# Kernel optimization log

Hardware: AMD Instinct MI355X
Metric: run time of the kernel (lower is better)

The kernel has to match this reference:

```python
import jax, jax.numpy as jnp
import numpy as np

HEADS = 16
EMBED = 1024
D_K = EMBED // HEADS


def setup_inputs() -> dict:
    key = jax.random.key(0)
    ks = jax.random.split(key, 11)
    B, S, E = 4, 2048, EMBED
    sc = 0.02
    return {
        "query": jax.random.normal(ks[0], (B, S, E), jnp.float32),
        "key_": jax.random.normal(ks[1], (B, S, E), jnp.float32),
        "value": jax.random.normal(ks[2], (B, S, E), jnp.float32),
        "Wq": jax.random.normal(ks[3], (E, E), jnp.float32) * sc,
        "bq": jnp.zeros((E,), jnp.float32),
        "Wk": jax.random.normal(ks[4], (E, E), jnp.float32) * sc,
        "bk": jnp.zeros((E,), jnp.float32),
        "Wv": jax.random.normal(ks[5], (E, E), jnp.float32) * sc,
        "bv": jnp.zeros((E,), jnp.float32),
        "Wo": jax.random.normal(ks[6], (E, D_K), jnp.float32) * sc,  # out: Linear(heads*d_k -> d_k)
        "bo": jnp.zeros((D_K,), jnp.float32),
    }


def reference(query, key_, value, Wq, bq, Wk, bk, Wv, bv, Wo, bo):
    B, S, E = query.shape
    H, Dk = HEADS, D_K
    # QKV projections
    q = query @ Wq + bq          # (B,S,E)
    k = key_ @ Wk + bk
    v = value @ Wv + bv
    # split heads -> (B,H,S,Dk)
    q = q.reshape(B, S, H, Dk).transpose(0, 2, 1, 3)
    k = k.reshape(B, S, H, Dk).transpose(0, 2, 1, 3)
    v = v.reshape(B, S, H, Dk).transpose(0, 2, 1, 3)
    # attention: softmax(QK^T / sqrt(d_k)) V
    scores = jnp.einsum("bhqd,bhkd->bhqk", q, k) / jnp.sqrt(jnp.asarray(Dk, q.dtype))
    attn = jax.nn.softmax(scores, axis=-1)
    ctx = jnp.einsum("bhqk,bhkd->bhqd", attn, v)
    ctx = ctx.transpose(0, 2, 1, 3).reshape(B, S, E)
    # output projection (E -> d_k, as in source)
    return ctx @ Wo + bo
```

## Files before the change

### kernel.cpp

```cpp
#include <hip/hip_runtime.h>
#include <hip/hip_bf16.h>
#include <cstdint>
#include <cstddef>

#define DEVI static __device__ __forceinline__

typedef unsigned short u16;
typedef unsigned int u32;
typedef __bf16 bf16_t;
typedef __bf16 bf16x8 __attribute__((ext_vector_type(8)));
typedef float f32x4 __attribute__((ext_vector_type(4)));
typedef float f32x16 __attribute__((ext_vector_type(16)));

union U16x8 { uint4 u; bf16x8 v; };
union PU { u32 w[4]; bf16x8 v; };

#define QSCALE 0.1803368801111204f

DEVI void gload_lds16(const void* g, void* l) {
  __builtin_amdgcn_global_load_lds((const __attribute__((address_space(1))) void*)g,
                                   (__attribute__((address_space(3))) void*)l, 16, 0, 0);
}
DEVI void wait_vmcnt0() { asm volatile("s_waitcnt vmcnt(0)" ::: "memory"); }

DEVI u32 cvt_pk_bf16(float lo, float hi) {
  u32 r;
  asm("v_cvt_pk_bf16_f32 %0, %1, %2" : "=v"(r) : "v"(lo), "v"(hi));
  return r;
}

DEVI void permswap(u32& a, u32& b) {
  asm("v_permlane32_swap_b32 %0, %1" : "+v"(a), "+v"(b));
}

DEVI f32x16 mfma32(bf16x8 a, bf16x8 b, f32x16 c) {
  return __builtin_amdgcn_mfma_f32_32x32x16_bf16(a, b, c, 0, 0, 0);
}

DEVI bf16x8 lds_frag(const char* base, int row, int koff, int swz) {
  U16x8 u;
  u.u = *(const uint4*)(base + row * 128 + (koff ^ swz));
  return u.v;
}

DEVI void transpose_body(const float* __restrict__ src, bf16_t* __restrict__ dst,
                         int R, int C, float scale, int tile, int t,
                         u16 (*tileb)[65]) {
  int tiles_c = C >> 6;
  int tc = tile % tiles_c;
  int tr = tile / tiles_c;
  int r0 = tr << 6, c0 = tc << 6;
  #pragma unroll
  for (int p = 0; p < 4; ++p) {
    int idx = t + p * 256;
    int i = idx >> 4, j4 = (idx & 15) * 4;
    float4 f = *(const float4*)(src + (size_t)(r0 + i) * C + c0 + j4);
    tileb[i][j4 + 0] = __builtin_bit_cast(u16, (bf16_t)(f.x * scale));
    tileb[i][j4 + 1] = __builtin_bit_cast(u16, (bf16_t)(f.y * scale));
    tileb[i][j4 + 2] = __builtin_bit_cast(u16, (bf16_t)(f.z * scale));
    tileb[i][j4 + 3] = __builtin_bit_cast(u16, (bf16_t)(f.w * scale));
  }
  __syncthreads();
  #pragma unroll
  for (int p = 0; p < 2; ++p) {
    int idx = t + p * 256;
    int j = idx >> 3, i0 = (idx & 7) * 8;
    u16 us[8];
    #pragma unroll
    for (int e = 0; e < 8; ++e) us[e] = tileb[i0 + e][j];
    uint4 o;
    o.x = (u32)us[0] | ((u32)us[1] << 16);
    o.y = (u32)us[2] | ((u32)us[3] << 16);
    o.z = (u32)us[4] | ((u32)us[5] << 16);
    o.w = (u32)us[6] | ((u32)us[7] << 16);
    *(uint4*)((u16*)dst + (size_t)(c0 + j) * R + r0 + i0) = o;
  }
}

__global__ __launch_bounds__(256) void k_prep(
    const float* __restrict__ qa, const float* __restrict__ ka, const float* __restrict__ va,
    const float* __restrict__ Wq, const float* __restrict__ Wk,
    const float* __restrict__ Wv, const float* __restrict__ Wo,
    bf16_t* __restrict__ Abf,
    bf16_t* __restrict__ WqT, bf16_t* __restrict__ WkT,
    bf16_t* __restrict__ WvT, bf16_t* __restrict__ WoT) {
  __shared__ u16 tileb[64][65];
  const int bid = blockIdx.x;
  const int t = threadIdx.x;
  if (bid < 3072) {
    int which = bid >> 10;
    int bb = bid & 1023;
    const float* s = which == 0 ? qa : which == 1 ? ka : va;
    u16* d = (u16*)Abf + (size_t)which * 8192 * 1024;
    size_t base = ((size_t)bb * 256 + t) * 8;
    #pragma unroll
    for (int p = 0; p < 4; ++p) {
      size_t i = base + (size_t)p * 2097152;
      float4 f0 = *(const float4*)(s + i);
      float4 f1 = *(const float4*)(s + i + 4);
      uint4 o;
      o.x = cvt_pk_bf16(f0.x, f0.y); o.y = cvt_pk_bf16(f0.z, f0.w);
      o.z = cvt_pk_bf16(f1.x, f1.y); o.w = cvt_pk_bf16(f1.z, f1.w);
      *(uint4*)(d + i) = o;
    }
  } else {
    int r = bid - 3072;
    if (r < 256)      transpose_body(Wq, WqT, 1024, 1024, QSCALE, r,       t, tileb);
    else if (r < 512) transpose_body(Wk, WkT, 1024, 1024, 1.0f,   r - 256, t, tileb);
    else if (r < 768) transpose_body(Wv, WvT, 1024, 1024, 1.0f,   r - 512, t, tileb);
    else              transpose_body(Wo, WoT, 1024, 64,   1.0f,   r - 768, t, tileb);
  }
}

template<bool PRE>
__global__ __launch_bounds__(256) void k_proj_gemm(
    const float* __restrict__ Aq, const float* __restrict__ Ak, const float* __restrict__ Av,
    const bf16_t* __restrict__ Abf,
    const bf16_t* __restrict__ WqT, const bf16_t* __restrict__ WkT, const bf16_t* __restrict__ WvT,
    const float* __restrict__ bq, const float* __restrict__ bk, const float* __restrict__ bv,
    bf16_t* __restrict__ qh, bf16_t* __restrict__ kh, bf16_t* __restrict__ vT) {
  int bx = blockIdx.x;
  int which = bx >> 9;
  int tt = bx & 511;
  int tile_m = tt & 63;
  int tile_n = tt >> 6;
  const float* A    = which == 0 ? Aq : which == 1 ? Ak : Av;
  const bf16_t* Ab  = Abf + (size_t)which * 8192 * 1024;
  const bf16_t* WT  = which == 0 ? WqT : which == 1 ? WkT : WvT;
  const float* bias = which == 0 ? bq : which == 1 ? bk : bv;
  const float bscale = which == 0 ? QSCALE : 1.0f;

  const int t = threadIdx.x;
  const int l = t & 63;
  const int w = t >> 6;
  const int wm = w >> 1, wn = w & 1;
  const int c = l & 15, g = l >> 4;
  const int row0 = tile_m << 7;
  const int n0 = tile_n << 7;

  __shared__ __align__(16) char As[128 * 64 * 2];
  __shared__ __align__(16) char Bs[128 * 64 * 2];

  f32x4 acc[4][4];
  #pragma unroll
  for (int i = 0; i < 4; ++i)
    #pragma unroll
    for (int j = 0; j < 4; ++j) acc[i][j] = (f32x4){0.f, 0.f, 0.f, 0.f};

  const int arow_b = t >> 4, ac4 = t & 15;
  const float* agbase = A + (size_t)(row0 + arow_b) * 1024 + ac4 * 4;
  char* aldst = As + arow_b * 128 + (((ac4 >> 1) ^ (arow_b & 7)) << 4) + (ac4 & 1) * 8;

  for (int kt = 0; kt < 16; ++kt) {
    __syncthreads();
    if constexpr (PRE) {
      #pragma unroll
      for (int cc = 0; cc < 4; ++cc) {
        int slot = w * 256 + cc * 64 + l;
        int row = slot >> 3, chs = slot & 7;
        const bf16_t* src = Ab + (size_t)(row0 + row) * 1024 + kt * 64 + ((chs ^ (row & 7)) << 3);
        gload_lds16(src, As + (w * 256 + cc * 64) * 16);
      }
    } else {
      const float* ap = agbase + kt * 64;
      #pragma unroll
      for (int p = 0; p < 8; ++p) {
        float4 f = *(const float4*)(ap + (size_t)p * 16384);
        uint2 o;
        o.x = cvt_pk_bf16(f.x, f.y);
        o.y = cvt_pk_bf16(f.z, f.w);
        *(uint2*)(aldst + p * 2048) = o;
      }
    }
    #pragma unroll
    for (int cc = 0; cc < 4; ++cc) {
      int slot = w * 256 + cc * 64 + l;
      int row = slot >> 3, chs = slot & 7;
      const bf16_t* src = WT + (size_t)(n0 + row) * 1024 + kt * 64 + ((chs ^ (row & 7)) << 3);
      gload_lds16(src, Bs + (w * 256 + cc * 64) * 16);
    }
    wait_vmcnt0();
    __syncthreads();
    #pragma unroll
    for (int kk = 0; kk < 2; ++kk) {
      bf16x8 af[4], bfr[4];
      #pragma unroll
      for (int mi = 0; mi < 4; ++mi) {
        int row = wm * 64 + mi * 16 + c;
        U16x8 u; u.u = *(const uint4*)(As + row * 128 + ((kk * 64 + g * 16) ^ ((c & 7) << 4)));
        af[mi] = u.v;
      }
      #pragma unroll
      for (int ni = 0; ni < 4; ++ni) {
        int row = wn * 64 + ni * 16 + c;
        U16x8 u; u.u = *(const uint4*)(Bs + row * 128 + ((kk * 64 + g * 16) ^ ((c & 7) << 4)));
        bfr[ni] = u.v;
      }
      #pragma unroll
      for (int mi = 0; mi < 4; ++mi)
        #pragma unroll
        for (int ni = 0; ni < 4; ++ni)
          acc[mi][ni] = __builtin_amdgcn_mfma_f32_16x16x32_bf16(af[mi], bfr[ni], acc[mi][ni], 0, 0, 0);
    }
  }

  const int b = row0 >> 11;
  const int sl0 = row0 & 2047;
  if (which == 2) {
    u16* vbase = (u16*)vT;
    #pragma unroll
    for (int ni = 0; ni < 4; ++ni) {
      int col = n0 + wn * 64 + ni * 16 + c;
      float bb = bias[col];
      int h = col >> 6, d = col & 63;
      u16* rowp = vbase + (((size_t)(b * 16 + h) * 64 + d) * 2048);
      #pragma unroll
      for (int mi = 0; mi < 4; ++mi) {
        int s = sl0 + wm * 64 + mi * 16 + g * 4;
        uint2 pv;
        pv.x = cvt_pk_bf16(acc[mi][ni][0] + bb, acc[mi][ni][1] + bb);
        pv.y = cvt_pk_bf16(acc[mi][ni][2] + bb, acc[mi][ni][3] + bb);
        *(uint2*)(rowp + s) = pv;
      }
    }
  } else {
    bf16_t* dst = which == 0 ? qh : kh;
    u16* dd = (u16*)dst;
    #pragma unroll
    for (int ni = 0; ni < 4; ++ni) {
      int col = n0 + wn * 64 + ni * 16 + c;
      float bb = bias[col] * bscale;
      int h = col >> 6, d = col & 63;
      #pragma unroll
      for (int mi = 0; mi < 4; ++mi) {
        #pragma unroll
        for (int r = 0; r < 4; ++r) {
          int s = sl0 + wm * 64 + mi * 16 + g * 4 + r;
          float vv = acc[mi][ni][r] + bb;
          size_t idx = (((size_t)b * 16 + h) * 2048 + s) * 64 + d;
          dd[idx] = __builtin_bit_cast(u16, (bf16_t)vv);
        }
      }
    }
  }
}

__global__ __launch_bounds__(256, 4) void k_attn(
    const bf16_t* __restrict__ qh, const bf16_t* __restrict__ kh,
    const bf16_t* __restrict__ vT, bf16_t* __restrict__ ctx) {
  const int bid = blockIdx.x;
  const int bx = ((bid & 7) << 7) | (bid >> 3);
  const int bh = bx >> 4;
  const int qt = bx & 15;
  const int q0 = qt << 7;
  const int t = threadIdx.x, l = t & 63, w = t >> 6;
  const int q = l & 31;
  const int hi = l >> 5;
  const int swz = (q & 7) << 4;

  __shared__ __align__(16) char Ks[2][64 * 128];
  __shared__ __align__(16) char Vs[2][64 * 128];

  const u16* qrow = (const u16*)qh + ((size_t)bh * 2048 + q0 + w * 32 + q) * 64;
  bf16x8 qf0, qf1, qf2, qf3;
  {
    U16x8 u;
    u.u = *(const uint4*)(qrow + 0 * 16 + hi * 8); qf0 = u.v;
    u.u = *(const uint4*)(qrow + 1 * 16 + hi * 8); qf1 = u.v;
    u.u = *(const uint4*)(qrow + 2 * 16 + hi * 8); qf2 = u.v;
    u.u = *(const uint4*)(qrow + 3 * 16 + hi * 8); qf3 = u.v;
  }

  bf16x8 ones;
  {
    U16x8 u;
    u.u = (uint4){0x3F803F80u, 0x3F803F80u, 0x3F803F80u, 0x3F803F80u};
    ones = u.v;
  }

  const f32x16 z16 = {0.f,0.f,0.f,0.f, 0.f,0.f,0.f,0.f, 0.f,0.f,0.f,0.f, 0.f,0.f,0.f,0.f};
  f32x16 oc0 = z16, oc1 = z16, psum = z16;

  const u16* kbh = (const u16*)kh + (size_t)bh * 2048 * 64;
  const u16* vbh = (const u16*)vT + (size_t)bh * 64 * 2048;

  auto stage = [&](int kvi, int buf) {
    int kbase = kvi << 6;
    #pragma unroll
    for (int cc = 0; cc < 2; ++cc) {
      int slot = w * 128 + cc * 64 + l;
      int row = slot >> 3, chs = slot & 7;
      gload_lds16(kbh + (size_t)(kbase + row) * 64 + ((chs ^ (row & 7)) << 3),
                  Ks[buf] + (w * 128 + cc * 64) * 16);
      gload_lds16(vbh + (size_t)row * 2048 + kbase + ((chs ^ (row & 7)) << 3),
                  Vs[buf] + (w * 128 + cc * 64) * 16);
    }
  };

  stage(0, 0);
  wait_vmcnt0();
  __syncthreads();

  for (int kv = 0; kv < 32; ++kv) {
    const int cur = kv & 1;
    if (kv < 31) stage(kv + 1, cur ^ 1);
    const char* Kc = Ks[cur];
    const char* Vc = Vs[cur];

    #pragma unroll
    for (int tt = 0; tt < 2; ++tt) {
      const int arow = tt * 32 + q;
      f32x16 st = z16;
      __builtin_amdgcn_s_setprio(1);
      st = mfma32(lds_frag(Kc, arow, 0 * 32 + hi * 16, swz), qf0, st);
      st = mfma32(lds_frag(Kc, arow, 1 * 32 + hi * 16, swz), qf1, st);
      st = mfma32(lds_frag(Kc, arow, 2 * 32 + hi * 16, swz), qf2, st);
      st = mfma32(lds_frag(Kc, arow, 3 * 32 + hi * 16, swz), qf3, st);
      __builtin_amdgcn_s_setprio(0);

      float e[16];
      #pragma unroll
      for (int i = 0; i < 16; ++i) e[i] = __builtin_amdgcn_exp2f(st[i]);

      #pragma unroll
      for (int cc = 0; cc < 2; ++cc) {
        u32 a  = cvt_pk_bf16(e[8 * cc + 0], e[8 * cc + 1]);
        u32 b  = cvt_pk_bf16(e[8 * cc + 4], e[8 * cc + 5]);
        u32 c2 = cvt_pk_bf16(e[8 * cc + 2], e[8 * cc + 3]);
        u32 d  = cvt_pk_bf16(e[8 * cc + 6], e[8 * cc + 7]);
        permswap(a, b);
        permswap(c2, d);
        PU pu;
        pu.w[0] = a; pu.w[1] = c2; pu.w[2] = b; pu.w[3] = d;
        const int ks = tt * 2 + cc;
        __builtin_amdgcn_s_setprio(1);
        oc0 = mfma32(pu.v, lds_frag(Vc, q,      ks * 32 + hi * 16, swz), oc0);
        oc1 = mfma32(pu.v, lds_frag(Vc, 32 + q, ks * 32 + hi * 16, swz), oc1);
        psum = mfma32(pu.v, ones, psum);
        __builtin_amdgcn_s_setprio(0);
      }
    }
    wait_vmcnt0();
    __syncthreads();
  }

  const int b = bh >> 4, hh = bh & 15;
  u16* cb = (u16*)ctx;
  #pragma unroll
  for (int qd = 0; qd < 4; ++qd) {
    #pragma unroll
    for (int r = 0; r < 4; ++r) {
      float inv = 1.f / psum[qd * 4 + r];
      int qrow_g = q0 + w * 32 + qd * 8 + hi * 4 + r;
      size_t base = ((size_t)b * 2048 + qrow_g) * 1024 + hh * 64;
      float v0 = oc0[qd * 4 + r] * inv;
      float v1 = oc1[qd * 4 + r] * inv;
      cb[base + q]      = __builtin_bit_cast(u16, (bf16_t)v0);
      cb[base + 32 + q] = __builtin_bit_cast(u16, (bf16_t)v1);
    }
  }
}

__global__ __launch_bounds__(256) void k_out_gemm(
    const bf16_t* __restrict__ ctx, const bf16_t* __restrict__ WoT,
    const float* __restrict__ bo, float* __restrict__ out) {
  int tile_m = blockIdx.x;
  const int t = threadIdx.x, l = t & 63, w = t >> 6;
  const int wm = w >> 1, wn = w & 1;
  const int c = l & 15, g = l >> 4;
  const int row0 = tile_m << 5;

  __shared__ __align__(16) char As[32 * 64 * 2];
  __shared__ __align__(16) char Bs[64 * 64 * 2];

  f32x4 acc[2];
  acc[0] = (f32x4){0.f, 0.f, 0.f, 0.f};
  acc[1] = (f32x4){0.f, 0.f, 0.f, 0.f};

  for (int kt = 0; kt < 16; ++kt) {
    __syncthreads();
    {
      int row = t >> 3, chs = t & 7;
      const bf16_t* src = ctx + (size_t)(row0 + row) * 1024 + kt * 64 + ((chs ^ (row & 7)) << 3);
      gload_lds16(src, As + t * 16);
    }
    #pragma unroll
    for (int cc = 0; cc < 2; ++cc) {
      int slot = w * 128 + cc * 64 + l;
      int row = slot >> 3, chs = slot & 7;
      const bf16_t* src = WoT + (size_t)row * 1024 + kt * 64 + ((chs ^ (row & 7)) << 3);
      gload_lds16(src, Bs + (w * 128 + cc * 64) * 16);
    }
    wait_vmcnt0();
    __syncthreads();
    #pragma unroll
    for (int kk = 0; kk < 2; ++kk) {
      bf16x8 af;
      {
        int row = wm * 16 + c;
        U16x8 u; u.u = *(const uint4*)(As + row * 128 + ((kk * 64 + g * 16) ^ ((c & 7) << 4)));
        af = u.v;
      }
      #pragma unroll
      for (int ni = 0; ni < 2; ++ni) {
        int row = wn * 32 + ni * 16 + c;
        U16x8 u; u.u = *(const uint4*)(Bs + row * 128 + ((kk * 64 + g * 16) ^ ((c & 7) << 4)));
        acc[ni] = __builtin_amdgcn_mfma_f32_16x16x32_bf16(af, u.v, acc[ni], 0, 0, 0);
      }
    }
  }
  #pragma unroll
  for (int ni = 0; ni < 2; ++ni) {
    int col = wn * 32 + ni * 16 + c;
    float bb = bo[col];
    #pragma unroll
    for (int r = 0; r < 4; ++r) {
      int rowg = row0 + wm * 16 + g * 4 + r;
      out[(size_t)rowg * 64 + col] = acc[ni][r] + bb;
    }
  }
}

extern "C" void kernel_launch(void* const* d_in, const int* in_sizes, int n_in,
                              void* d_out, int out_size, void* d_ws, size_t ws_size,
                              hipStream_t stream) {
  (void)in_sizes; (void)n_in; (void)out_size;
  const float* query = (const float*)d_in[0];
  const float* key_  = (const float*)d_in[1];
  const float* value = (const float*)d_in[2];
  const float* Wq = (const float*)d_in[3];
  const float* bq = (const float*)d_in[4];
  const float* Wk = (const float*)d_in[5];
  const float* bk = (const float*)d_in[6];
  const float* Wv = (const float*)d_in[7];
  const float* bv = (const float*)d_in[8];
  const float* Wo = (const float*)d_in[9];
  const float* bo = (const float*)d_in[10];
  float* out = (float*)d_out;

  char* ws = (char*)d_ws;
  bf16_t* WqT = (bf16_t*)(ws + (size_t)0);
  bf16_t* WkT = (bf16_t*)(ws + ((size_t)2 << 20));
  bf16_t* WvT = (bf16_t*)(ws + ((size_t)4 << 20));
  bf16_t* WoT = (bf16_t*)(ws + ((size_t)6 << 20));
  bf16_t* qhd = (bf16_t*)(ws + ((size_t)8 << 20));
  bf16_t* khd = (bf16_t*)(ws + ((size_t)24 << 20));
  bf16_t* vT  = (bf16_t*)(ws + ((size_t)56 << 20));
  bf16_t* ctx = (bf16_t*)(ws + ((size_t)72 << 20));
  bf16_t* Abf = (bf16_t*)(ws + ((size_t)88 << 20));

  const bool pre = ws_size >= ((size_t)137 << 20);

  k_prep<<<3856, 256, 0, stream>>>(query, key_, value, Wq, Wk, Wv, Wo,
                                   Abf, WqT, WkT, WvT, WoT);
  if (pre) {
    k_proj_gemm<true><<<1536, 256, 0, stream>>>(query, key_, value, Abf, WqT, WkT, WvT,
                                                bq, bk, bv, qhd, khd, vT);
  } else {
    k_proj_gemm<false><<<1536, 256, 0, stream>>>(query, key_, value, Abf, WqT, WkT, WvT,
                                                 bq, bk, bv, qhd, khd, vT);
  }
  k_attn<<<1024, 256, 0, stream>>>(qhd, khd, vT, ctx);
  k_out_gemm<<<256, 256, 0, stream>>>(ctx, WoT, bo, out);
}
```

Measured before the change: 186.4 us.

## Double attention block size and KV tile to reuse staged K/V across more queries

The attention kernel now uses 512 threads per block covering 256 query rows, so each staged K/V tile is shared by twice as many query rows. It also loads 128 keys per stage instead of 64, which halves the number of loop iterations and barriers. LDS per block grows to 64 KB, and the V tile uses a 256-byte row stride with a swizzle that only covers the low 8 chunks. The risks are lower occupancy, fewer blocks than the original grid (512), and LDS bank conflicts on the wider V rows.

```diff
diff --git a/kernel.cpp b/kernel.cpp
--- a/kernel.cpp
+++ b/kernel.cpp
@@ -37,9 +37,10 @@
   return __builtin_amdgcn_mfma_f32_32x32x16_bf16(a, b, c, 0, 0, 0);
 }
 
+template<int STRIDE>
 DEVI bf16x8 lds_frag(const char* base, int row, int koff, int swz) {
   U16x8 u;
-  u.u = *(const uint4*)(base + row * 128 + (koff ^ swz));
+  u.u = *(const uint4*)(base + row * STRIDE + (koff ^ swz));
   return u.v;
 }
 
@@ -245,21 +246,21 @@
   }
 }
 
-__global__ __launch_bounds__(256, 4) void k_attn(
+__global__ __launch_bounds__(512, 4) void k_attn(
     const bf16_t* __restrict__ qh, const bf16_t* __restrict__ kh,
     const bf16_t* __restrict__ vT, bf16_t* __restrict__ ctx) {
   const int bid = blockIdx.x;
-  const int bx = ((bid & 7) << 7) | (bid >> 3);
-  const int bh = bx >> 4;
-  const int qt = bx & 15;
-  const int q0 = qt << 7;
+  const int bx = ((bid & 7) << 6) | (bid >> 3);
+  const int bh = bx >> 3;
+  const int qt = bx & 7;
+  const int q0 = qt << 8;
   const int t = threadIdx.x, l = t & 63, w = t >> 6;
   const int q = l & 31;
   const int hi = l >> 5;
   const int swz = (q & 7) << 4;
 
-  __shared__ __align__(16) char Ks[2][64 * 128];
-  __shared__ __align__(16) char Vs[2][64 * 128];
+  __shared__ __align__(16) char Ks[2][128 * 128];
+  __shared__ __align__(16) char Vs[2][64 * 256];
 
   const u16* qrow = (const u16*)qh + ((size_t)bh * 2048 + q0 + w * 32 + q) * 64;
   bf16x8 qf0, qf1, qf2, qf3;
@@ -285,15 +286,21 @@
   const u16* vbh = (const u16*)vT + (size_t)bh * 64 * 2048;
 
   auto stage = [&](int kvi, int buf) {
-    int kbase = kvi << 6;
+    int kbase = kvi << 7;
     #pragma unroll
     for (int cc = 0; cc < 2; ++cc) {
-      int slot = w * 128 + cc * 64 + l;
-      int row = slot >> 3, chs = slot & 7;
-      gload_lds16(kbh + (size_t)(kbase + row) * 64 + ((chs ^ (row & 7)) << 3),
-                  Ks[buf] + (w * 128 + cc * 64) * 16);
-      gload_lds16(vbh + (size_t)row * 2048 + kbase + ((chs ^ (row & 7)) << 3),
-                  Vs[buf] + (w * 128 + cc * 64) * 16);
+      int slot = cc * 512 + t;
+      {
+        int row = slot >> 3, chs = slot & 7;
+        gload_lds16(kbh + (size_t)(kbase + row) * 64 + ((chs ^ (row & 7)) << 3),
+                    Ks[buf] + (cc * 512 + w * 64) * 16);
+      }
+      {
+        int row = slot >> 4, chs = slot & 15;
+        int chsw = (chs & 8) | ((chs & 7) ^ (row & 7));
+        gload_lds16(vbh + (size_t)row * 2048 + kbase + (chsw << 3),
+                    Vs[buf] + (cc * 512 + w * 64) * 16);
+      }
     }
   };
 
@@ -301,21 +308,21 @@
   wait_vmcnt0();
   __syncthreads();
 
-  for (int kv = 0; kv < 32; ++kv) {
+  for (int kv = 0; kv < 16; ++kv) {
     const int cur = kv & 1;
-    if (kv < 31) stage(kv + 1, cur ^ 1);
+    if (kv < 15) stage(kv + 1, cur ^ 1);
     const char* Kc = Ks[cur];
     const char* Vc = Vs[cur];
 
     #pragma unroll
-    for (int tt = 0; tt < 2; ++tt) {
+    for (int tt = 0; tt < 4; ++tt) {
       const int arow = tt * 32 + q;
       f32x16 st = z16;
       __builtin_amdgcn_s_setprio(1);
-      st = mfma32(lds_frag(Kc, arow, 0 * 32 + hi * 16, swz), qf0, st);
-      st = mfma32(lds_frag(Kc, arow, 1 * 32 + hi * 16, swz), qf1, st);
-      st = mfma32(lds_frag(Kc, arow, 2 * 32 + hi * 16, swz), qf2, st);
-      st = mfma32(lds_frag(Kc, arow, 3 * 32 + hi * 16, swz), qf3, st);
+      st = mfma32(lds_frag<128>(Kc, arow, 0 * 32 + hi * 16, swz), qf0, st);
+      st = mfma32(lds_frag<128>(Kc, arow, 1 * 32 + hi * 16, swz), qf1, st);
+      st = mfma32(lds_frag<128>(Kc, arow, 2 * 32 + hi * 16, swz), qf2, st);
+      st = mfma32(lds_frag<128>(Kc, arow, 3 * 32 + hi * 16, swz), qf3, st);
       __builtin_amdgcn_s_setprio(0);
 
       float e[16];
@@ -333,9 +340,10 @@
         PU pu;
         pu.w[0] = a; pu.w[1] = c2; pu.w[2] = b; pu.w[3] = d;
         const int ks = tt * 2 + cc;
+        const int koff = ks * 32 + hi * 16;
         __builtin_amdgcn_s_setprio(1);
-        oc0 = mfma32(pu.v, lds_frag(Vc, q,      ks * 32 + hi * 16, swz), oc0);
-        oc1 = mfma32(pu.v, lds_frag(Vc, 32 + q, ks * 32 + hi * 16, swz), oc1);
+        oc0 = mfma32(pu.v, lds_frag<256>(Vc, q,      koff, swz), oc0);
+        oc1 = mfma32(pu.v, lds_frag<256>(Vc, 32 + q, koff, swz), oc1);
         psum = mfma32(pu.v, ones, psum);
         __builtin_amdgcn_s_setprio(0);
       }
@@ -460,6 +468,6 @@
     k_proj_gemm<false><<<1536, 256, 0, stream>>>(query, key_, value, Abf, WqT, WkT, WvT,
                                                  bq, bk, bv, qhd, khd, vT);
   }
-  k_attn<<<1024, 256, 0, stream>>>(qhd, khd, vT, ctx);
+  k_attn<<<512, 512, 0, stream>>>(qhd, khd, vT, ctx);
   k_out_gemm<<<256, 256, 0, stream>>>(ctx, WoT, bo, out);
 }
```

New measurement: 180.4 us (median of 3 runs). 3.2% less time.
